# Kernel tuning notes

Hardware: AMD Instinct MI355X
Metric: run time of the kernel (lower is better)

Reference implementation:

```python
import jax, jax.numpy as jnp
import numpy as np

B, L, C_IN, D, H, DFF, NL, NC, PH = 32, 512, 16, 512, 8, 2048, 3, 10, 128
DH = D // H


def circ_conv1d(x, w):
    # x: [B, C, S] with circular padding 1 on spatial dim, w: [O, C, 3]
    xp = jnp.concatenate([x[..., -1:], x, x[..., :1]], axis=-1)
    return jax.lax.conv_general_dilated(xp, w, (1,), 'VALID',
                                        dimension_numbers=('NCH', 'OIH', 'NCH'))


def positional_embedding(length, d):
    pos = jnp.arange(length, dtype=jnp.float32)[:, None]
    div = jnp.exp(jnp.arange(0, d, 2, dtype=jnp.float32) * (-np.log(10000.0) / d))
    pe = jnp.zeros((length, d), jnp.float32)
    pe = pe.at[:, 0::2].set(jnp.sin(pos * div))
    pe = pe.at[:, 1::2].set(jnp.cos(pos * div))
    return pe


def layer_norm(x, g, b):
    m = jnp.mean(x, -1, keepdims=True)
    v = jnp.var(x, -1, keepdims=True)
    return (x - m) / jnp.sqrt(v + 1e-5) * g + b


def projector(x, stats, conv_w, w0, b0, w1, b1, w2):
    # x: [B, L, C_IN] (channels = seq_len, spatial = enc_in), stats: [B, 1, C_IN]
    y = circ_conv1d(x, conv_w)                     # [B, 1, C_IN]
    y = jnp.concatenate([y, stats], axis=1)        # [B, 2, C_IN]
    y = y.reshape(x.shape[0], -1)                  # [B, 2*C_IN]
    h = jax.nn.relu(y @ w0.T + b0)
    h = jax.nn.relu(h @ w1.T + b1)
    return h @ w2.T                                # no bias on output


def setup_inputs() -> dict:
    key = jax.random.key(0)
    ks = iter(jax.random.split(key, 64))
    rn = lambda shape, s=0.02: jax.random.normal(next(ks), shape, jnp.float32) * s
    inp = {
        'x_enc': jax.random.normal(next(ks), (B, L, C_IN), jnp.float32),
        'x_mark_enc': jnp.ones((B, L), jnp.float32),
        'tok_w': rn((D, C_IN, 3)),
        'Wq': rn((NL, D, D)), 'bq': jnp.zeros((NL, D)),
        'Wk': rn((NL, D, D)), 'bk': jnp.zeros((NL, D)),
        'Wv': rn((NL, D, D)), 'bv': jnp.zeros((NL, D)),
        'Wo': rn((NL, D, D)), 'bo': jnp.zeros((NL, D)),
        'W1': rn((NL, DFF, D)), 'b1': jnp.zeros((NL, DFF)),
        'W2': rn((NL, D, DFF)), 'b2': jnp.zeros((NL, D)),
        'ln1_g': jnp.ones((NL, D)), 'ln1_b': jnp.zeros((NL, D)),
        'ln2_g': jnp.ones((NL, D)), 'ln2_b': jnp.zeros((NL, D)),
        'norm_g': jnp.ones((D,)), 'norm_b': jnp.zeros((D,)),
        'proj_w': rn((NC, D * L)), 'proj_b': jnp.zeros((NC,)),
        'tau_conv_w': rn((1, L, 3)), 'tau_w0': rn((PH, 2 * C_IN)), 'tau_b0': jnp.zeros((PH,)),
        'tau_w1': rn((PH, PH)), 'tau_b1': jnp.zeros((PH,)), 'tau_w2': rn((1, PH)),
        'del_conv_w': rn((1, L, 3)), 'del_w0': rn((PH, 2 * C_IN)), 'del_b0': jnp.zeros((PH,)),
        'del_w1': rn((PH, PH)), 'del_b1': jnp.zeros((PH,)), 'del_w2': rn((L, PH)),
    }
    return inp


def reference(x_enc, x_mark_enc, tok_w,
              Wq, bq, Wk, bk, Wv, bv, Wo, bo,
              W1, b1, W2, b2, ln1_g, ln1_b, ln2_g, ln2_b,
              norm_g, norm_b, proj_w, proj_b,
              tau_conv_w, tau_w0, tau_b0, tau_w1, tau_b1, tau_w2,
              del_conv_w, del_w0, del_b0, del_w1, del_b1, del_w2):
    # De-stationary statistics (detached in the original)
    x_raw = jax.lax.stop_gradient(x_enc)
    mean_enc = jnp.mean(x_raw, 1, keepdims=True)                 # [B,1,C]
    std_enc = jnp.sqrt(jnp.var(x_raw, 1, keepdims=True) + 1e-5)  # [B,1,C]
    tau = jnp.exp(projector(x_raw, std_enc, tau_conv_w, tau_w0, tau_b0,
                            tau_w1, tau_b1, tau_w2))             # [B,1]
    delta = projector(x_raw, mean_enc, del_conv_w, del_w0, del_b0,
                      del_w1, del_b1, del_w2)                    # [B,L]

    # DataEmbedding: circular token conv + sinusoidal positional encoding
    tok = circ_conv1d(jnp.transpose(x_enc, (0, 2, 1)), tok_w)    # [B,D,L]
    x = jnp.transpose(tok, (0, 2, 1)) + positional_embedding(L, D)[None]

    scale = 1.0 / np.sqrt(DH)
    tau4 = tau.reshape(B, 1, 1, 1)
    delta4 = delta[:, None, None, :]
    for i in range(NL):
        q = (x @ Wq[i].T + bq[i]).reshape(B, L, H, DH)
        k = (x @ Wk[i].T + bk[i]).reshape(B, L, H, DH)
        v = (x @ Wv[i].T + bv[i]).reshape(B, L, H, DH)
        scores = jnp.einsum('blhe,bshe->bhls', q, k) * tau4 + delta4
        A = jax.nn.softmax(scale * scores, axis=-1)
        o = jnp.einsum('bhls,bshd->blhd', A, v).reshape(B, L, D)
        o = o @ Wo[i].T + bo[i]
        x = layer_norm(x + o, ln1_g[i], ln1_b[i])
        y = jax.nn.gelu(x @ W1[i].T + b1[i], approximate=False) @ W2[i].T + b2[i]
        x = layer_norm(x + y, ln2_g[i], ln2_b[i])
    x = layer_norm(x, norm_g, norm_b)

    out = jax.nn.gelu(x, approximate=False)
    out = out * x_mark_enc[..., None]
    out = out.reshape(B, -1) @ proj_w.T + proj_b                 # [B, NC]
    return out
```

## Files before the change

kernel.cpp:

```cpp
#include <hip/hip_runtime.h>
#include <hip/hip_bf16.h>
#include <cstdint>

#define DEVINL __device__ __forceinline__

typedef unsigned short u16;
typedef short bf16x8 __attribute__((ext_vector_type(8)));
typedef float f32x4 __attribute__((ext_vector_type(4)));

DEVINL u16 f2b(float f) {
    union { float f; uint32_t u; } x{f};
    uint32_t r = x.u + 0x7fffu + ((x.u >> 16) & 1u);
    return (u16)(r >> 16);
}
DEVINL float b2f(u16 h) {
    union { uint32_t u; float f; } x{(uint32_t)h << 16};
    return x.f;
}
DEVINL float gelu_exact(float v) {
    return 0.5f * v * (1.0f + erff(v * 0.70710678118654752f));
}
DEVINL void gload_lds16(const void* g, void* l) {
    __builtin_amdgcn_global_load_lds(
        (const __attribute__((address_space(1))) void*)(uintptr_t)g,
        (__attribute__((address_space(3))) void*)(uint32_t)(uintptr_t)l,
        16, 0, 0);
}

__global__ void f2b_kernel(const float* __restrict__ in, u16* __restrict__ out, int n) {
    int i = (blockIdx.x * 256 + threadIdx.x) * 8;
    if (i + 8 <= n) {
        float4 a = *(const float4*)(in + i);
        float4 b = *(const float4*)(in + i + 4);
        u16 t[8] = {f2b(a.x), f2b(a.y), f2b(a.z), f2b(a.w),
                    f2b(b.x), f2b(b.y), f2b(b.z), f2b(b.w)};
        *(uint4*)(out + i) = *(const uint4*)t;
    }
}

__global__ void packb_kernel(const float* __restrict__ bq, const float* __restrict__ bk,
                             const float* __restrict__ bv, float* __restrict__ out) {
    int idx = blockIdx.x * 256 + threadIdx.x;
    if (idx >= 3 * 1536) return;
    int i = idx / 1536, j = idx - i * 1536;
    float v = (j < 512) ? bq[i * 512 + j]
            : (j < 1024) ? bk[i * 512 + j - 512]
                         : bv[i * 512 + j - 1024];
    out[idx] = v;
}

__global__ void pe_kernel(float* __restrict__ pet) {
    int l = blockIdx.x, d2 = threadIdx.x;
    float freq = expf(-(float)(2 * d2) * 0.0179889460390f);
    float ang = (float)l * freq;
    pet[l * 512 + 2 * d2]     = sinf(ang);
    pet[l * 512 + 2 * d2 + 1] = cosf(ang);
}

__global__ void stats_kernel(const float* __restrict__ xe, float* __restrict__ mean,
                             float* __restrict__ stdv) {
    int b = blockIdx.x, ln = threadIdx.x;
    int c = ln & 15, part = ln >> 4;
    float s = 0.f, sq = 0.f;
    for (int l = part; l < 512; l += 4) {
        float x = xe[(size_t)b * 8192 + l * 16 + c];
        s += x; sq += x * x;
    }
    s += __shfl_xor(s, 16);  s += __shfl_xor(s, 32);
    sq += __shfl_xor(sq, 16); sq += __shfl_xor(sq, 32);
    if (part == 0) {
        float m = s * (1.0f / 512.0f);
        mean[b * 16 + c] = m;
        stdv[b * 16 + c] = sqrtf(sq * (1.0f / 512.0f) - m * m + 1e-5f);
    }
}

__global__ __launch_bounds__(128)
void proj_kernel(const float* __restrict__ xe, const float* __restrict__ stats,
                 const float* __restrict__ cw, const float* __restrict__ w0,
                 const float* __restrict__ b0, const float* __restrict__ w1,
                 const float* __restrict__ b1, const float* __restrict__ w2,
                 float* __restrict__ outp, int outn, int do_exp) {
    __shared__ float zl[32], h0l[128], h1l[128], red[2];
    int b = blockIdx.x, tid = threadIdx.x;
    {
        int c = tid >> 3, part = tid & 7;
        float acc = 0.f;
        for (int l = part; l < 512; l += 8) {
            const float* xr = xe + (size_t)b * 8192 + l * 16;
            float w0v = cw[l * 3 + 0], w1v = cw[l * 3 + 1], w2v = cw[l * 3 + 2];
            acc += xr[(c + 15) & 15] * w0v + xr[c] * w1v + xr[(c + 1) & 15] * w2v;
        }
        acc += __shfl_xor(acc, 1); acc += __shfl_xor(acc, 2); acc += __shfl_xor(acc, 4);
        if (part == 0) zl[c] = acc;
        if (tid < 16) zl[16 + tid] = stats[b * 16 + tid];
    }
    __syncthreads();
    {
        float acc = b0[tid];
        #pragma unroll
        for (int i = 0; i < 32; ++i) acc += zl[i] * w0[tid * 32 + i];
        h0l[tid] = fmaxf(acc, 0.0f);
    }
    __syncthreads();
    {
        float acc = b1[tid];
        for (int i = 0; i < 128; ++i) acc += h0l[i] * w1[tid * 128 + i];
        h1l[tid] = fmaxf(acc, 0.0f);
    }
    __syncthreads();
    if (outn == 1) {
        float p = h1l[tid] * w2[tid];
        p += __shfl_xor(p, 1);  p += __shfl_xor(p, 2);  p += __shfl_xor(p, 4);
        p += __shfl_xor(p, 8);  p += __shfl_xor(p, 16); p += __shfl_xor(p, 32);
        if ((tid & 63) == 0) red[tid >> 6] = p;
        __syncthreads();
        if (tid == 0) {
            float v = red[0] + red[1];
            outp[b] = do_exp ? expf(v) : v;
        }
    } else {
        for (int l = tid; l < outn; l += 128) {
            float acc = 0.f;
            for (int i = 0; i < 128; ++i) acc += h1l[i] * w2[l * 128 + i];
            outp[(size_t)b * outn + l] = acc;
        }
    }
}

__global__ __launch_bounds__(256)
void tokconv_kernel(const float* __restrict__ xe, const float* __restrict__ tw,
                    const float* __restrict__ pet,
                    float* __restrict__ xf, u16* __restrict__ xb) {
    __shared__ float xs[34][16];
    int lt = blockIdx.x, b = blockIdx.y, tid = threadIdx.x;
    int l0 = lt * 32;
    for (int idx = tid; idx < 34 * 16; idx += 256) {
        int r = idx >> 4, c = idx & 15;
        int gl = (l0 - 1 + r + 512) & 511;
        xs[r][c] = xe[(size_t)b * 8192 + gl * 16 + c];
    }
    __syncthreads();
    for (int dd = tid; dd < 512; dd += 256) {
        float twr[48];
        #pragma unroll
        for (int i = 0; i < 48; ++i) twr[i] = tw[dd * 48 + i];
        for (int l = 0; l < 32; ++l) {
            float acc = 0.f;
            #pragma unroll
            for (int c = 0; c < 16; ++c) {
                acc += xs[l][c]     * twr[c * 3 + 0];
                acc += xs[l + 1][c] * twr[c * 3 + 1];
                acc += xs[l + 2][c] * twr[c * 3 + 2];
            }
            float vv = acc + pet[(size_t)(l0 + l) * 512 + dd];
            size_t idx = ((size_t)b * 512 + l0 + l) * 512 + dd;
            xf[idx] = vv;
            xb[idx] = f2b(vv);
        }
    }
}

template <int ACT, int OBF>
__global__ __launch_bounds__(256)
void gemm_bt(const u16* __restrict__ A, const u16* __restrict__ B,
             const float* __restrict__ bias, void* __restrict__ Cv0,
             u16* __restrict__ Cv1, int M, int N, int K, int Kc) {
    __shared__ u16 smem[3][2][128 * 32];
    const int tid = threadIdx.x, wv = tid >> 6, ln = tid & 63;
    const int nwg = gridDim.x * gridDim.y;
    const int bid = blockIdx.y * gridDim.x + blockIdx.x;
    const int wg  = (bid & 7) * (nwg >> 3) + (bid >> 3);
    const int n0 = (wg % gridDim.x) * 128;
    const int m0 = (wg / gridDim.x) * 128;
    const int kz = blockIdx.z;
    const int wm = (wv >> 1) * 64, wn = (wv & 1) * 64;
    const int lo = ln & 15, hi = ln >> 4;
    f32x4 acc[4][4] = {};
    const int r0 = wv * 16 + (ln >> 2);
    const int sl = ln & 3;
    const int k0 = kz * Kc;

    auto stage = [&](int buf, int kt) {
        #pragma unroll
        for (int c = 0; c < 2; ++c) {
            int row = r0 + c * 64;
            int ssl = sl ^ ((row >> 1) & 3);
            int ldsoff = row * 32 + sl * 8;
            gload_lds16(A + (size_t)(m0 + row) * K + kt + ssl * 8, (char*)smem[buf][0] + ldsoff * 2);
            gload_lds16(B + (size_t)(n0 + row) * K + kt + ssl * 8, (char*)smem[buf][1] + ldsoff * 2);
        }
    };

    const int nt = Kc >> 5;
    stage(0, k0);
    if (nt > 1) stage(1, k0 + 32);
    for (int t = 0; t < nt; ++t) {
        if (t + 1 < nt) { asm volatile("s_waitcnt vmcnt(4)" ::: "memory"); }
        else            { asm volatile("s_waitcnt vmcnt(0)" ::: "memory"); }
        __builtin_amdgcn_s_barrier();
        if (t + 2 < nt) stage((t + 2) % 3, k0 + (t + 2) * 32);
        const u16* As = smem[t % 3][0];
        const u16* Bs = smem[t % 3][1];
        bf16x8 af[4], bfr[4];
        #pragma unroll
        for (int i = 0; i < 4; ++i) {
            int row = wm + i * 16 + lo;
            int slot = hi ^ ((row >> 1) & 3);
            af[i] = *(const bf16x8*)(As + row * 32 + slot * 8);
        }
        #pragma unroll
        for (int j = 0; j < 4; ++j) {
            int row = wn + j * 16 + lo;
            int slot = hi ^ ((row >> 1) & 3);
            bfr[j] = *(const bf16x8*)(Bs + row * 32 + slot * 8);
        }
        #pragma unroll
        for (int i = 0; i < 4; ++i)
            #pragma unroll
            for (int j = 0; j < 4; ++j)
                acc[i][j] = __builtin_amdgcn_mfma_f32_16x16x32_bf16(af[i], bfr[j], acc[i][j], 0, 0, 0);
    }
    __syncthreads();

    const bool second = (kz != 0);
    float* ep = (float*)smem + wv * (16 * 68);
    #pragma unroll
    for (int i = 0; i < 4; ++i) {
        #pragma unroll
        for (int j = 0; j < 4; ++j) {
            int col = n0 + wn + j * 16 + lo;
            float bv = second ? 0.0f : bias[col];
            #pragma unroll
            for (int r = 0; r < 4; ++r) {
                float v = acc[i][j][r] + bv;
                if (ACT == 1 && !second) v = gelu_exact(v);
                ep[(hi * 4 + r) * 68 + j * 16 + lo] = v;
            }
        }
        #pragma unroll
        for (int pp = 0; pp < 4; ++pp) {
            int rl = pp * 4 + hi;
            float4 vv = *(const float4*)(ep + rl * 68 + lo * 4);
            size_t row = (size_t)(m0 + wm + i * 16 + rl);
            int col = n0 + wn + lo * 4;
            if (second) {
                u16 t4[4] = {f2b(vv.x), f2b(vv.y), f2b(vv.z), f2b(vv.w)};
                *(uint2*)(Cv1 + row * N + col) = *(const uint2*)t4;
            } else if (OBF) {
                u16 t4[4] = {f2b(vv.x), f2b(vv.y), f2b(vv.z), f2b(vv.w)};
                *(uint2*)((u16*)Cv0 + row * N + col) = *(const uint2*)t4;
            } else {
                *(float4*)((float*)Cv0 + row * N + col) = vv;
            }
        }
    }
}

__global__ __launch_bounds__(512)
void attn2_kernel(const u16* __restrict__ qkv, const float* __restrict__ tau,
                  const float* __restrict__ delta, u16* __restrict__ o) {
    __shared__ u16 KL[64 * 64];
    __shared__ u16 VT[64 * 72];
    __shared__ u16 PL[8][32 * 64];
    const int tid = threadIdx.x, w = tid >> 6, ln = tid & 63;
    const int lo = ln & 15, hi = ln >> 4;
    const int qh = blockIdx.x, h = blockIdx.y, b = blockIdx.z;
    const size_t qrow0 = (size_t)b * 512;
    const u16* qp = qkv;
    const u16* kp = qkv + 512;
    const u16* vp = qkv + 1024;
    const int hofs = h * 64;
    const float ts = tau[b] * 0.125f;
    u16* Pw = (u16*)PL[w];
    const int q0 = qh * 256 + w * 32;

    bf16x8 qa[2][2];
    #pragma unroll
    for (int i = 0; i < 2; ++i)
        #pragma unroll
        for (int ks = 0; ks < 2; ++ks)
            qa[i][ks] = *(const bf16x8*)(qp + (qrow0 + q0 + i * 16 + lo) * 1536 + hofs + ks * 32 + hi * 8);

    float m_run[2] = {-1e30f, -1e30f};
    float l_run[2] = {0.f, 0.f};
    f32x4 oacc[2][4] = {};

    const int vsl = tid & 7, vsr = tid >> 3;
    uint4 vreg = *(const uint4*)(vp + (qrow0 + vsr) * 1536 + hofs + vsl * 8);

    for (int nt = 0; nt < 8; ++nt) {
        __syncthreads();
        {
            int s = tid >> 3, j = tid & 7;
            int jl = j ^ (s & 7);
            gload_lds16(kp + (qrow0 + nt * 64 + s) * 1536 + hofs + jl * 8,
                        (char*)KL + tid * 16);
        }
        {
            u16 tmp[8]; *(uint4*)tmp = vreg;
            #pragma unroll
            for (int e = 0; e < 8; ++e) {
                int d = vsl * 8 + e;
                int byt = d * 144 + (((vsr >> 3) ^ vsl) << 4) + (vsr & 7) * 2;
                *(u16*)((char*)VT + byt) = tmp[e];
            }
        }
        if (nt < 7)
            vreg = *(const uint4*)(vp + (qrow0 + (nt + 1) * 64 + vsr) * 1536 + hofs + vsl * 8);
        __syncthreads();

        f32x4 sacc[2][4] = {};
        #pragma unroll
        for (int ks = 0; ks < 2; ++ks) {
            #pragma unroll
            for (int jn = 0; jn < 4; ++jn) {
                int s = jn * 16 + lo;
                int phys = (ks * 4 + hi) ^ (s & 7);
                bf16x8 kb = *(const bf16x8*)((const char*)KL + s * 128 + phys * 16);
                #pragma unroll
                for (int i = 0; i < 2; ++i)
                    sacc[i][jn] = __builtin_amdgcn_mfma_f32_16x16x32_bf16(kb, qa[i][ks], sacc[i][jn], 0, 0, 0);
            }
        }
        float tmax[2] = {-1e30f, -1e30f};
        #pragma unroll
        for (int jn = 0; jn < 4; ++jn) {
            float4 dv4 = *(const float4*)(delta + b * 512 + nt * 64 + jn * 16 + hi * 4);
            float dv[4] = {dv4.x, dv4.y, dv4.z, dv4.w};
            #pragma unroll
            for (int i = 0; i < 2; ++i)
                #pragma unroll
                for (int r = 0; r < 4; ++r) {
                    float v = sacc[i][jn][r] * ts + dv[r] * 0.125f;
                    sacc[i][jn][r] = v;
                    tmax[i] = fmaxf(tmax[i], v);
                }
        }
        #pragma unroll
        for (int i = 0; i < 2; ++i) {
            tmax[i] = fmaxf(tmax[i], __shfl_xor(tmax[i], 16));
            tmax[i] = fmaxf(tmax[i], __shfl_xor(tmax[i], 32));
            float mnew = fmaxf(m_run[i], tmax[i]);
            float fac = __expf(m_run[i] - mnew);
            m_run[i] = mnew;
            l_run[i] *= fac;
            #pragma unroll
            for (int jd = 0; jd < 4; ++jd)
                #pragma unroll
                for (int r = 0; r < 4; ++r) oacc[i][jd][r] *= fac;
        }
        #pragma unroll
        for (int i = 0; i < 2; ++i) {
            float ls = 0.f;
            #pragma unroll
            for (int jn = 0; jn < 4; ++jn) {
                float p0 = __expf(sacc[i][jn][0] - m_run[i]);
                float p1 = __expf(sacc[i][jn][1] - m_run[i]);
                float p2 = __expf(sacc[i][jn][2] - m_run[i]);
                float p3 = __expf(sacc[i][jn][3] - m_run[i]);
                ls += (p0 + p1) + (p2 + p3);
                uint2 pk;
                pk.x = (uint32_t)f2b(p0) | ((uint32_t)f2b(p1) << 16);
                pk.y = (uint32_t)f2b(p2) | ((uint32_t)f2b(p3) << 16);
                int q = i * 16 + lo;
                int ls16 = jn * 2 + (hi >> 1);
                int byt = q * 128 + (((ls16 ^ (q & 7)) << 4)) + (hi & 1) * 8;
                *(uint2*)((char*)Pw + byt) = pk;
            }
            ls += __shfl_xor(ls, 16);
            ls += __shfl_xor(ls, 32);
            l_run[i] += ls;
        }
        #pragma unroll
        for (int ks2 = 0; ks2 < 2; ++ks2) {
            bf16x8 pa[2];
            #pragma unroll
            for (int i = 0; i < 2; ++i) {
                int q = i * 16 + lo;
                int phys = (ks2 * 4 + hi) ^ (q & 7);
                pa[i] = *(const bf16x8*)((const char*)Pw + q * 128 + phys * 16);
            }
            #pragma unroll
            for (int jd = 0; jd < 4; ++jd) {
                int d = jd * 16 + lo;
                int cs = (ks2 * 4 + hi) ^ ((d >> 3) & 7);
                bf16x8 vb = *(const bf16x8*)((const char*)VT + d * 144 + cs * 16);
                #pragma unroll
                for (int i = 0; i < 2; ++i)
                    oacc[i][jd] = __builtin_amdgcn_mfma_f32_16x16x32_bf16(vb, pa[i], oacc[i][jd], 0, 0, 0);
            }
        }
    }
    #pragma unroll
    for (int i = 0; i < 2; ++i) {
        float inv = 1.0f / l_run[i];
        #pragma unroll
        for (int jd = 0; jd < 4; ++jd) {
            u16 t4[4];
            #pragma unroll
            for (int r = 0; r < 4; ++r) t4[r] = f2b(oacc[i][jd][r] * inv);
            size_t row = qrow0 + q0 + i * 16 + lo;
            *(uint2*)(o + row * 512 + hofs + jd * 16 + hi * 4) = *(const uint2*)t4;
        }
    }
}

__global__ __launch_bounds__(256)
void ln3_kernel(const float* __restrict__ xin, const float* __restrict__ res0,
                const u16* res1, const float* __restrict__ g,
                const float* __restrict__ bta,
                float* __restrict__ xout, u16* xbf) {
    const int row = blockIdx.x * 4 + (threadIdx.x >> 6);
    const int ln = threadIdx.x & 63;
    const float* xr = xin + (size_t)row * 512;
    const float* rr = res0 + (size_t)row * 512;
    const u16* pr = res1 + (size_t)row * 512;
    float4 a = *(const float4*)(xr + ln * 4);
    float4 c = *(const float4*)(xr + 256 + ln * 4);
    float4 ra = *(const float4*)(rr + ln * 4);
    float4 rc = *(const float4*)(rr + 256 + ln * 4);
    uint2 pa_ = *(const uint2*)(pr + ln * 4);
    uint2 pc_ = *(const uint2*)(pr + 256 + ln * 4);
    const u16* pa16 = (const u16*)&pa_;
    const u16* pc16 = (const u16*)&pc_;
    a.x += ra.x + b2f(pa16[0]); a.y += ra.y + b2f(pa16[1]);
    a.z += ra.z + b2f(pa16[2]); a.w += ra.w + b2f(pa16[3]);
    c.x += rc.x + b2f(pc16[0]); c.y += rc.y + b2f(pc16[1]);
    c.z += rc.z + b2f(pc16[2]); c.w += rc.w + b2f(pc16[3]);
    float s = a.x + a.y + a.z + a.w + c.x + c.y + c.z + c.w;
    float sq = a.x*a.x + a.y*a.y + a.z*a.z + a.w*a.w + c.x*c.x + c.y*c.y + c.z*c.z + c.w*c.w;
    #pragma unroll
    for (int m = 1; m < 64; m <<= 1) { s += __shfl_xor(s, m); sq += __shfl_xor(sq, m); }
    float mean = s * 0.001953125f;
    float var = sq * 0.001953125f - mean * mean;
    float rstd = rsqrtf(var + 1e-5f);
    float4 g0 = *(const float4*)(g + ln * 4);
    float4 g1 = *(const float4*)(g + 256 + ln * 4);
    float4 b0 = *(const float4*)(bta + ln * 4);
    float4 b1 = *(const float4*)(bta + 256 + ln * 4);
    float4 o0, o1;
    o0.x = (a.x - mean) * rstd * g0.x + b0.x;
    o0.y = (a.y - mean) * rstd * g0.y + b0.y;
    o0.z = (a.z - mean) * rstd * g0.z + b0.z;
    o0.w = (a.w - mean) * rstd * g0.w + b0.w;
    o1.x = (c.x - mean) * rstd * g1.x + b1.x;
    o1.y = (c.y - mean) * rstd * g1.y + b1.y;
    o1.z = (c.z - mean) * rstd * g1.z + b1.z;
    o1.w = (c.w - mean) * rstd * g1.w + b1.w;
    *(float4*)(xout + (size_t)row * 512 + ln * 4) = o0;
    *(float4*)(xout + (size_t)row * 512 + 256 + ln * 4) = o1;
    u16 t0[4] = {f2b(o0.x), f2b(o0.y), f2b(o0.z), f2b(o0.w)};
    u16 t1[4] = {f2b(o1.x), f2b(o1.y), f2b(o1.z), f2b(o1.w)};
    *(uint2*)(xbf + (size_t)row * 512 + ln * 4) = *(const uint2*)t0;
    *(uint2*)(xbf + (size_t)row * 512 + 256 + ln * 4) = *(const uint2*)t1;
}

__global__ __launch_bounds__(256)
void lngelu_kernel(const float* __restrict__ xin, const float* __restrict__ g,
                   const float* __restrict__ bta, const float* __restrict__ mark,
                   u16* __restrict__ outb) {
    const int row = blockIdx.x * 4 + (threadIdx.x >> 6);
    const int ln = threadIdx.x & 63;
    const float* xr = xin + (size_t)row * 512;
    float4 a = *(const float4*)(xr + ln * 4);
    float4 c = *(const float4*)(xr + 256 + ln * 4);
    float s = a.x + a.y + a.z + a.w + c.x + c.y + c.z + c.w;
    float sq = a.x*a.x + a.y*a.y + a.z*a.z + a.w*a.w + c.x*c.x + c.y*c.y + c.z*c.z + c.w*c.w;
    #pragma unroll
    for (int m = 1; m < 64; m <<= 1) { s += __shfl_xor(s, m); sq += __shfl_xor(sq, m); }
    float mean = s * 0.001953125f;
    float var = sq * 0.001953125f - mean * mean;
    float rstd = rsqrtf(var + 1e-5f);
    float mk = mark[row];
    float4 g0 = *(const float4*)(g + ln * 4);
    float4 g1 = *(const float4*)(g + 256 + ln * 4);
    float4 b0 = *(const float4*)(bta + ln * 4);
    float4 b1 = *(const float4*)(bta + 256 + ln * 4);
    float v0 = gelu_exact((a.x - mean) * rstd * g0.x + b0.x) * mk;
    float v1 = gelu_exact((a.y - mean) * rstd * g0.y + b0.y) * mk;
    float v2 = gelu_exact((a.z - mean) * rstd * g0.z + b0.z) * mk;
    float v3 = gelu_exact((a.w - mean) * rstd * g0.w + b0.w) * mk;
    float v4 = gelu_exact((c.x - mean) * rstd * g1.x + b1.x) * mk;
    float v5 = gelu_exact((c.y - mean) * rstd * g1.y + b1.y) * mk;
    float v6 = gelu_exact((c.z - mean) * rstd * g1.z + b1.z) * mk;
    float v7 = gelu_exact((c.w - mean) * rstd * g1.w + b1.w) * mk;
    u16 t0[4] = {f2b(v0), f2b(v1), f2b(v2), f2b(v3)};
    u16 t1[4] = {f2b(v4), f2b(v5), f2b(v6), f2b(v7)};
    *(uint2*)(outb + (size_t)row * 512 + ln * 4) = *(const uint2*)t0;
    *(uint2*)(outb + (size_t)row * 512 + 256 + ln * 4) = *(const uint2*)t1;
}

__global__ __launch_bounds__(256)
void fproj_kernel(const u16* __restrict__ gb, const u16* __restrict__ pw,
                  const float* __restrict__ pb, float* __restrict__ out) {
    __shared__ float red[32][4];
    int n = blockIdx.x, ks = blockIdx.y, tid = threadIdx.x;
    float acc[32];
    #pragma unroll
    for (int m = 0; m < 32; ++m) acc[m] = 0.f;
    for (int j = 0; j < 8; ++j) {
        size_t k0 = (size_t)ks * 16384 + j * 2048 + tid * 8;
        bf16x8 w8 = *(const bf16x8*)(pw + (size_t)n * 262144 + k0);
        float wf[8];
        #pragma unroll
        for (int e = 0; e < 8; ++e) wf[e] = b2f((u16)w8[e]);
        #pragma unroll
        for (int m = 0; m < 32; ++m) {
            bf16x8 g8 = *(const bf16x8*)(gb + (size_t)m * 262144 + k0);
            float a = acc[m];
            #pragma unroll
            for (int e = 0; e < 8; ++e) a += b2f((u16)g8[e]) * wf[e];
            acc[m] = a;
        }
    }
    int w = tid >> 6;
    #pragma unroll
    for (int m = 0; m < 32; ++m) {
        float s = acc[m];
        s += __shfl_xor(s, 1);  s += __shfl_xor(s, 2);  s += __shfl_xor(s, 4);
        s += __shfl_xor(s, 8);  s += __shfl_xor(s, 16); s += __shfl_xor(s, 32);
        if ((tid & 63) == 0) red[m][w] = s;
    }
    __syncthreads();
    if (tid < 32) {
        int m = tid;
        float s = red[m][0] + red[m][1] + red[m][2] + red[m][3];
        if (ks == 0) s += pb[n];
        atomicAdd(&out[m * 10 + n], s);
    }
}

extern "C" void kernel_launch(void* const* d_in, const int* in_sizes, int n_in,
                              void* d_out, int out_size, void* d_ws, size_t ws_size,
                              hipStream_t stream) {
    const float* x_enc  = (const float*)d_in[0];
    const float* x_mark = (const float*)d_in[1];
    const float* tok_w  = (const float*)d_in[2];
    const float* Wq = (const float*)d_in[3];   const float* bq = (const float*)d_in[4];
    const float* Wk = (const float*)d_in[5];   const float* bk = (const float*)d_in[6];
    const float* Wv = (const float*)d_in[7];   const float* bv = (const float*)d_in[8];
    const float* Wo = (const float*)d_in[9];   const float* bo = (const float*)d_in[10];
    const float* W1 = (const float*)d_in[11];  const float* b1 = (const float*)d_in[12];
    const float* W2 = (const float*)d_in[13];  const float* b2 = (const float*)d_in[14];
    const float* ln1_g = (const float*)d_in[15]; const float* ln1_b = (const float*)d_in[16];
    const float* ln2_g = (const float*)d_in[17]; const float* ln2_b = (const float*)d_in[18];
    const float* norm_g = (const float*)d_in[19]; const float* norm_b = (const float*)d_in[20];
    const float* proj_w = (const float*)d_in[21]; const float* proj_b = (const float*)d_in[22];
    const float* tau_cw = (const float*)d_in[23];
    const float* tau_w0 = (const float*)d_in[24]; const float* tau_b0 = (const float*)d_in[25];
    const float* tau_w1 = (const float*)d_in[26]; const float* tau_b1 = (const float*)d_in[27];
    const float* tau_w2 = (const float*)d_in[28];
    const float* del_cw = (const float*)d_in[29];
    const float* del_w0 = (const float*)d_in[30]; const float* del_b0 = (const float*)d_in[31];
    const float* del_w1 = (const float*)d_in[32]; const float* del_b1 = (const float*)d_in[33];
    const float* del_w2 = (const float*)d_in[34];
    float* out = (float*)d_out;

    char* ws = (char*)d_ws;
    size_t off = 0;
    auto alloc = [&](size_t bytes) -> void* {
        void* p = ws + off;
        off += (bytes + 255) & ~(size_t)255;
        return p;
    };
    u16* wqkvb = (u16*)alloc((size_t)3 * 786432 * 2);
    u16* wob = (u16*)alloc(786432 * 2);
    u16* w1b = (u16*)alloc(3145728 * 2);
    u16* w2b = (u16*)alloc(3145728 * 2);
    u16* pwb = (u16*)alloc(2621440 * 2);
    float* bqkvb = (float*)alloc(3 * 1536 * 4);
    float* petab = (float*)alloc((size_t)262144 * 4);
    float* meanb = (float*)alloc(512 * 4);
    float* stdb  = (float*)alloc(512 * 4);
    float* taub  = (float*)alloc(32 * 4);
    float* delb  = (float*)alloc(16384 * 4);
    float* xf = (float*)alloc((size_t)8388608 * 4);
    u16*  xb  = (u16*)alloc((size_t)8388608 * 2);
    float* sf = (float*)alloc((size_t)8388608 * 4);
    u16* qkvb = (u16*)alloc((size_t)16384 * 1536 * 2);
    u16* ob   = (u16*)alloc((size_t)8388608 * 2);
    u16* hb   = qkvb;
    u16* gbuf = qkvb;
    u16* p1o  = qkvb;
    u16* p1f  = xb;

    auto cvt = [&](const float* src, u16* dst, int n) {
        f2b_kernel<<<dim3((n + 2047) / 2048), dim3(256), 0, stream>>>(src, dst, n);
    };
    for (int i = 0; i < 3; ++i) {
        cvt(Wq + (size_t)i * 262144, wqkvb + (size_t)i * 786432 + 0,      262144);
        cvt(Wk + (size_t)i * 262144, wqkvb + (size_t)i * 786432 + 262144, 262144);
        cvt(Wv + (size_t)i * 262144, wqkvb + (size_t)i * 786432 + 524288, 262144);
    }
    cvt(Wo, wob, 786432);
    cvt(W1, w1b, 3145728); cvt(W2, w2b, 3145728);
    cvt(proj_w, pwb, 2621440);
    packb_kernel<<<dim3(18), dim3(256), 0, stream>>>(bq, bk, bv, bqkvb);
    pe_kernel<<<dim3(512), dim3(256), 0, stream>>>(petab);

    stats_kernel<<<dim3(32), dim3(64), 0, stream>>>(x_enc, meanb, stdb);
    proj_kernel<<<dim3(32), dim3(128), 0, stream>>>(x_enc, stdb, tau_cw, tau_w0, tau_b0,
                                                    tau_w1, tau_b1, tau_w2, taub, 1, 1);
    proj_kernel<<<dim3(32), dim3(128), 0, stream>>>(x_enc, meanb, del_cw, del_w0, del_b0,
                                                    del_w1, del_b1, del_w2, delb, 512, 0);
    tokconv_kernel<<<dim3(16, 32), dim3(256), 0, stream>>>(x_enc, tok_w, petab, xf, xb);

    for (int i = 0; i < 3; ++i) {
        const u16* wqkv_i = wqkvb + (size_t)i * 786432;
        const u16* wo_i = wob + (size_t)i * 262144;
        const u16* w1_i = w1b + (size_t)i * 1048576;
        const u16* w2_i = w2b + (size_t)i * 1048576;
        gemm_bt<0, 1><<<dim3(12, 128, 1), dim3(256), 0, stream>>>(
            xb, wqkv_i, bqkvb + i * 1536, qkvb, nullptr, 16384, 1536, 512, 512);
        attn2_kernel<<<dim3(2, 8, 32), dim3(512), 0, stream>>>(qkvb, taub, delb, ob);
        gemm_bt<0, 0><<<dim3(4, 128, 2), dim3(256), 0, stream>>>(
            ob, wo_i, bo + i * 512, sf, p1o, 16384, 512, 512, 256);
        ln3_kernel<<<dim3(4096), dim3(256), 0, stream>>>(xf, sf, p1o,
            ln1_g + i * 512, ln1_b + i * 512, xf, xb);
        gemm_bt<1, 1><<<dim3(16, 128, 1), dim3(256), 0, stream>>>(
            xb, w1_i, b1 + i * 2048, hb, nullptr, 16384, 2048, 512, 512);
        gemm_bt<0, 0><<<dim3(4, 128, 2), dim3(256), 0, stream>>>(
            hb, w2_i, b2 + i * 512, sf, p1f, 16384, 512, 2048, 1024);
        ln3_kernel<<<dim3(4096), dim3(256), 0, stream>>>(xf, sf, p1f,
            ln2_g + i * 512, ln2_b + i * 512, xf, xb);
    }

    lngelu_kernel<<<dim3(4096), dim3(256), 0, stream>>>(xf, norm_g, norm_b, x_mark, gbuf);
    hipMemsetAsync(d_out, 0, (size_t)out_size * 4, stream);
    fproj_kernel<<<dim3(10, 16), dim3(256), 0, stream>>>(gbuf, pwb, proj_b, out);
}
```

Before: 1.001 ms.

## Switch GEMMs to 32x32x16 MFMA, bf16 split-K partials, fuse weight conversions

The GEMM kernel now uses 32x32x16 bf16 MFMA tiles (2x2 per wave) instead of 16x16x32, which reduces LDS fragment reads per MFMA. The first split-K partial is also stored as bf16 instead of fp32, halving that buffer's traffic into the layernorm kernel at some precision cost. The many per-tensor weight conversion launches are merged into two kernels to cut launch overhead. The memory clobbers on the waitcnt asm were also dropped, which risks compiler reordering around the LDS pipeline.

```diff
diff --git a/kernel.cpp b/kernel.cpp
--- a/kernel.cpp
+++ b/kernel.cpp
@@ -7,6 +7,7 @@
 typedef unsigned short u16;
 typedef short bf16x8 __attribute__((ext_vector_type(8)));
 typedef float f32x4 __attribute__((ext_vector_type(4)));
+typedef float f32x16 __attribute__((ext_vector_type(16)));
 
 DEVINL u16 f2b(float f) {
     union { float f; uint32_t u; } x{f};
@@ -26,16 +27,38 @@
         (__attribute__((address_space(3))) void*)(uint32_t)(uintptr_t)l,
         16, 0, 0);
 }
-
-__global__ void f2b_kernel(const float* __restrict__ in, u16* __restrict__ out, int n) {
-    int i = (blockIdx.x * 256 + threadIdx.x) * 8;
-    if (i + 8 <= n) {
-        float4 a = *(const float4*)(in + i);
-        float4 b = *(const float4*)(in + i + 4);
-        u16 t[8] = {f2b(a.x), f2b(a.y), f2b(a.z), f2b(a.w),
-                    f2b(b.x), f2b(b.y), f2b(b.z), f2b(b.w)};
-        *(uint4*)(out + i) = *(const uint4*)t;
-    }
+DEVINL void cvt8(const float* src, u16* dst) {
+    float4 a = *(const float4*)src;
+    float4 b = *(const float4*)(src + 4);
+    u16 t[8] = {f2b(a.x), f2b(a.y), f2b(a.z), f2b(a.w),
+                f2b(b.x), f2b(b.y), f2b(b.z), f2b(b.w)};
+    *(uint4*)dst = *(const uint4*)t;
+}
+
+__global__ __launch_bounds__(256)
+void cvtqkv_kernel(const float* __restrict__ Wq, const float* __restrict__ Wk,
+                   const float* __restrict__ Wv, u16* __restrict__ dst) {
+    size_t i = ((size_t)blockIdx.x * 256 + threadIdx.x) * 8;
+    int slice = (int)(i >> 18);
+    int layer = slice / 3, which = slice - layer * 3;
+    size_t rem = i & 262143;
+    const float* src = (which == 0 ? Wq : which == 1 ? Wk : Wv) + (size_t)layer * 262144 + rem;
+    u16* d = dst + (size_t)layer * 786432 + (size_t)which * 262144 + rem;
+    cvt8(src, d);
+}
+__global__ __launch_bounds__(256)
+void cvt4_kernel(const float* __restrict__ s0, const float* __restrict__ s1,
+                 const float* __restrict__ s2, const float* __restrict__ s3,
+                 u16* __restrict__ d0, u16* __restrict__ d1,
+                 u16* __restrict__ d2, u16* __restrict__ d3) {
+    size_t i = ((size_t)blockIdx.x * 256 + threadIdx.x) * 8;
+    if (i < 786432) { cvt8(s0 + i, d0 + i); return; }
+    i -= 786432;
+    if (i < 3145728) { cvt8(s1 + i, d1 + i); return; }
+    i -= 3145728;
+    if (i < 3145728) { cvt8(s2 + i, d2 + i); return; }
+    i -= 3145728;
+    if (i < 2621440) { cvt8(s3 + i, d3 + i); }
 }
 
 __global__ void packb_kernel(const float* __restrict__ bq, const float* __restrict__ bk,
@@ -161,11 +184,11 @@
     }
 }
 
-template <int ACT, int OBF>
+template <int ACT>
 __global__ __launch_bounds__(256)
-void gemm_bt(const u16* __restrict__ A, const u16* __restrict__ B,
-             const float* __restrict__ bias, void* __restrict__ Cv0,
-             u16* __restrict__ Cv1, int M, int N, int K, int Kc) {
+void gemm32(const u16* __restrict__ A, const u16* __restrict__ B,
+            const float* __restrict__ bias, u16* __restrict__ Cv0,
+            u16* __restrict__ Cv1, int M, int N, int K, int Kc) {
     __shared__ u16 smem[3][2][128 * 32];
     const int tid = threadIdx.x, wv = tid >> 6, ln = tid & 63;
     const int nwg = gridDim.x * gridDim.y;
@@ -175,16 +198,16 @@
     const int m0 = (wg / gridDim.x) * 128;
     const int kz = blockIdx.z;
     const int wm = (wv >> 1) * 64, wn = (wv & 1) * 64;
-    const int lo = ln & 15, hi = ln >> 4;
-    f32x4 acc[4][4] = {};
-    const int r0 = wv * 16 + (ln >> 2);
+    const int l31 = ln & 31, h2 = ln >> 5;
+    f32x16 acc[2][2] = {};
+    const int r0s = wv * 16 + (ln >> 2);
     const int sl = ln & 3;
     const int k0 = kz * Kc;
 
     auto stage = [&](int buf, int kt) {
         #pragma unroll
         for (int c = 0; c < 2; ++c) {
-            int row = r0 + c * 64;
+            int row = r0s + c * 64;
             int ssl = sl ^ ((row >> 1) & 3);
             int ldsoff = row * 32 + sl * 8;
             gload_lds16(A + (size_t)(m0 + row) * K + kt + ssl * 8, (char*)smem[buf][0] + ldsoff * 2);
@@ -196,63 +219,73 @@
     stage(0, k0);
     if (nt > 1) stage(1, k0 + 32);
     for (int t = 0; t < nt; ++t) {
-        if (t + 1 < nt) { asm volatile("s_waitcnt vmcnt(4)" ::: "memory"); }
-        else            { asm volatile("s_waitcnt vmcnt(0)" ::: "memory"); }
+        if (t + 1 < nt) { asm volatile("s_waitcnt vmcnt(4)"); }
+        else            { asm volatile("s_waitcnt vmcnt(0)"); }
         __builtin_amdgcn_s_barrier();
         if (t + 2 < nt) stage((t + 2) % 3, k0 + (t + 2) * 32);
         const u16* As = smem[t % 3][0];
         const u16* Bs = smem[t % 3][1];
-        bf16x8 af[4], bfr[4];
-        #pragma unroll
-        for (int i = 0; i < 4; ++i) {
-            int row = wm + i * 16 + lo;
-            int slot = hi ^ ((row >> 1) & 3);
-            af[i] = *(const bf16x8*)(As + row * 32 + slot * 8);
-        }
-        #pragma unroll
-        for (int j = 0; j < 4; ++j) {
-            int row = wn + j * 16 + lo;
-            int slot = hi ^ ((row >> 1) & 3);
-            bfr[j] = *(const bf16x8*)(Bs + row * 32 + slot * 8);
-        }
-        #pragma unroll
-        for (int i = 0; i < 4; ++i)
-            #pragma unroll
-            for (int j = 0; j < 4; ++j)
-                acc[i][j] = __builtin_amdgcn_mfma_f32_16x16x32_bf16(af[i], bfr[j], acc[i][j], 0, 0, 0);
+        bf16x8 af[2][2], bfr[2][2];
+        #pragma unroll
+        for (int mi = 0; mi < 2; ++mi) {
+            int row = wm + mi * 32 + l31;
+            int swz = (row >> 1) & 3;
+            #pragma unroll
+            for (int kk = 0; kk < 2; ++kk) {
+                int phys = (kk * 2 + h2) ^ swz;
+                af[mi][kk] = *(const bf16x8*)(As + row * 32 + phys * 8);
+            }
+        }
+        #pragma unroll
+        for (int nj = 0; nj < 2; ++nj) {
+            int row = wn + nj * 32 + l31;
+            int swz = (row >> 1) & 3;
+            #pragma unroll
+            for (int kk = 0; kk < 2; ++kk) {
+                int phys = (kk * 2 + h2) ^ swz;
+                bfr[nj][kk] = *(const bf16x8*)(Bs + row * 32 + phys * 8);
+            }
+        }
+        #pragma unroll
+        for (int mi = 0; mi < 2; ++mi)
+            #pragma unroll
+            for (int nj = 0; nj < 2; ++nj)
+                #pragma unroll
+                for (int kk = 0; kk < 2; ++kk)
+                    acc[mi][nj] = __builtin_amdgcn_mfma_f32_32x32x16_bf16(
+                        af[mi][kk], bfr[nj][kk], acc[mi][nj], 0, 0, 0);
     }
     __syncthreads();
 
     const bool second = (kz != 0);
-    float* ep = (float*)smem + wv * (16 * 68);
+    float* eps = (float*)smem + wv * (16 * 68);
+    u16* Cout = second ? Cv1 : Cv0;
     #pragma unroll
-    for (int i = 0; i < 4; ++i) {
-        #pragma unroll
-        for (int j = 0; j < 4; ++j) {
-            int col = n0 + wn + j * 16 + lo;
-            float bv = second ? 0.0f : bias[col];
-            #pragma unroll
-            for (int r = 0; r < 4; ++r) {
-                float v = acc[i][j][r] + bv;
-                if (ACT == 1 && !second) v = gelu_exact(v);
-                ep[(hi * 4 + r) * 68 + j * 16 + lo] = v;
-            }
+    for (int ch = 0; ch < 4; ++ch) {
+        const int mi = ch >> 1, rsel = ch & 1;
+        #pragma unroll
+        for (int nj = 0; nj < 2; ++nj) {
+            int col = nj * 32 + l31;
+            float bv = second ? 0.0f : bias[n0 + wn + col];
+            #pragma unroll
+            for (int r1l = 0; r1l < 2; ++r1l)
+                #pragma unroll
+                for (int rr = 0; rr < 4; ++rr) {
+                    int reg = rr + 4 * (rsel * 2 + r1l);
+                    int rloc = h2 * 4 + rr + 8 * r1l;
+                    float v = acc[mi][nj][reg] + bv;
+                    if (ACT == 1 && !second) v = gelu_exact(v);
+                    eps[rloc * 68 + col] = v;
+                }
         }
         #pragma unroll
         for (int pp = 0; pp < 4; ++pp) {
-            int rl = pp * 4 + hi;
-            float4 vv = *(const float4*)(ep + rl * 68 + lo * 4);
-            size_t row = (size_t)(m0 + wm + i * 16 + rl);
-            int col = n0 + wn + lo * 4;
-            if (second) {
-                u16 t4[4] = {f2b(vv.x), f2b(vv.y), f2b(vv.z), f2b(vv.w)};
-                *(uint2*)(Cv1 + row * N + col) = *(const uint2*)t4;
-            } else if (OBF) {
-                u16 t4[4] = {f2b(vv.x), f2b(vv.y), f2b(vv.z), f2b(vv.w)};
-                *(uint2*)((u16*)Cv0 + row * N + col) = *(const uint2*)t4;
-            } else {
-                *(float4*)((float*)Cv0 + row * N + col) = vv;
-            }
+            int rl = pp * 4 + (ln >> 4);
+            float4 vv = *(const float4*)(eps + rl * 68 + (ln & 15) * 4);
+            size_t row = (size_t)(m0 + wm + ch * 16 + rl);
+            int col = n0 + wn + (ln & 15) * 4;
+            u16 t4[4] = {f2b(vv.x), f2b(vv.y), f2b(vv.z), f2b(vv.w)};
+            *(uint2*)(Cout + row * N + col) = *(const uint2*)t4;
         }
     }
 }
@@ -407,27 +440,27 @@
 }
 
 __global__ __launch_bounds__(256)
-void ln3_kernel(const float* __restrict__ xin, const float* __restrict__ res0,
+void ln3_kernel(const float* __restrict__ xin, const u16* res0,
                 const u16* res1, const float* __restrict__ g,
                 const float* __restrict__ bta,
                 float* __restrict__ xout, u16* xbf) {
     const int row = blockIdx.x * 4 + (threadIdx.x >> 6);
     const int ln = threadIdx.x & 63;
     const float* xr = xin + (size_t)row * 512;
-    const float* rr = res0 + (size_t)row * 512;
-    const u16* pr = res1 + (size_t)row * 512;
+    const u16* r0p = res0 + (size_t)row * 512;
+    const u16* r1p = res1 + (size_t)row * 512;
     float4 a = *(const float4*)(xr + ln * 4);
     float4 c = *(const float4*)(xr + 256 + ln * 4);
-    float4 ra = *(const float4*)(rr + ln * 4);
-    float4 rc = *(const float4*)(rr + 256 + ln * 4);
-    uint2 pa_ = *(const uint2*)(pr + ln * 4);
-    uint2 pc_ = *(const uint2*)(pr + 256 + ln * 4);
-    const u16* pa16 = (const u16*)&pa_;
-    const u16* pc16 = (const u16*)&pc_;
-    a.x += ra.x + b2f(pa16[0]); a.y += ra.y + b2f(pa16[1]);
-    a.z += ra.z + b2f(pa16[2]); a.w += ra.w + b2f(pa16[3]);
-    c.x += rc.x + b2f(pc16[0]); c.y += rc.y + b2f(pc16[1]);
-    c.z += rc.z + b2f(pc16[2]); c.w += rc.w + b2f(pc16[3]);
+    uint2 qa_ = *(const uint2*)(r0p + ln * 4);
+    uint2 qc_ = *(const uint2*)(r0p + 256 + ln * 4);
+    uint2 pa_ = *(const uint2*)(r1p + ln * 4);
+    uint2 pc_ = *(const uint2*)(r1p + 256 + ln * 4);
+    const u16* qa16 = (const u16*)&qa_;  const u16* qc16 = (const u16*)&qc_;
+    const u16* pa16 = (const u16*)&pa_;  const u16* pc16 = (const u16*)&pc_;
+    a.x += b2f(qa16[0]) + b2f(pa16[0]); a.y += b2f(qa16[1]) + b2f(pa16[1]);
+    a.z += b2f(qa16[2]) + b2f(pa16[2]); a.w += b2f(qa16[3]) + b2f(pa16[3]);
+    c.x += b2f(qc16[0]) + b2f(pc16[0]); c.y += b2f(qc16[1]) + b2f(pc16[1]);
+    c.z += b2f(qc16[2]) + b2f(pc16[2]); c.w += b2f(qc16[3]) + b2f(pc16[3]);
     float s = a.x + a.y + a.z + a.w + c.x + c.y + c.z + c.w;
     float sq = a.x*a.x + a.y*a.y + a.z*a.z + a.w*a.w + c.x*c.x + c.y*c.y + c.z*c.z + c.w*c.w;
     #pragma unroll
@@ -577,7 +610,7 @@
     float* delb  = (float*)alloc(16384 * 4);
     float* xf = (float*)alloc((size_t)8388608 * 4);
     u16*  xb  = (u16*)alloc((size_t)8388608 * 2);
-    float* sf = (float*)alloc((size_t)8388608 * 4);
+    u16*  sfb = (u16*)alloc((size_t)8388608 * 2);
     u16* qkvb = (u16*)alloc((size_t)16384 * 1536 * 2);
     u16* ob   = (u16*)alloc((size_t)8388608 * 2);
     u16* hb   = qkvb;
@@ -585,17 +618,8 @@
     u16* p1o  = qkvb;
     u16* p1f  = xb;
 
-    auto cvt = [&](const float* src, u16* dst, int n) {
-        f2b_kernel<<<dim3((n + 2047) / 2048), dim3(256), 0, stream>>>(src, dst, n);
-    };
-    for (int i = 0; i < 3; ++i) {
-        cvt(Wq + (size_t)i * 262144, wqkvb + (size_t)i * 786432 + 0,      262144);
-        cvt(Wk + (size_t)i * 262144, wqkvb + (size_t)i * 786432 + 262144, 262144);
-        cvt(Wv + (size_t)i * 262144, wqkvb + (size_t)i * 786432 + 524288, 262144);
-    }
-    cvt(Wo, wob, 786432);
-    cvt(W1, w1b, 3145728); cvt(W2, w2b, 3145728);
-    cvt(proj_w, pwb, 2621440);
+    cvtqkv_kernel<<<dim3(1152), dim3(256), 0, stream>>>(Wq, Wk, Wv, wqkvb);
+    cvt4_kernel<<<dim3(5030), dim3(256), 0, stream>>>(Wo, W1, W2, proj_w, wob, w1b, w2b, pwb);
     packb_kernel<<<dim3(18), dim3(256), 0, stream>>>(bq, bk, bv, bqkvb);
     pe_kernel<<<dim3(512), dim3(256), 0, stream>>>(petab);
 
@@ -611,18 +635,18 @@
         const u16* wo_i = wob + (size_t)i * 262144;
         const u16* w1_i = w1b + (size_t)i * 1048576;
         const u16* w2_i = w2b + (size_t)i * 1048576;
-        gemm_bt<0, 1><<<dim3(12, 128, 1), dim3(256), 0, stream>>>(
+        gemm32<0><<<dim3(12, 128, 1), dim3(256), 0, stream>>>(
             xb, wqkv_i, bqkvb + i * 1536, qkvb, nullptr, 16384, 1536, 512, 512);
         attn2_kernel<<<dim3(2, 8, 32), dim3(512), 0, stream>>>(qkvb, taub, delb, ob);
-        gemm_bt<0, 0><<<dim3(4, 128, 2), dim3(256), 0, stream>>>(
-            ob, wo_i, bo + i * 512, sf, p1o, 16384, 512, 512, 256);
-        ln3_kernel<<<dim3(4096), dim3(256), 0, stream>>>(xf, sf, p1o,
+        gemm32<0><<<dim3(4, 128, 2), dim3(256), 0, stream>>>(
+            ob, wo_i, bo + i * 512, sfb, p1o, 16384, 512, 512, 256);
+        ln3_kernel<<<dim3(4096), dim3(256), 0, stream>>>(xf, sfb, p1o,
             ln1_g + i * 512, ln1_b + i * 512, xf, xb);
-        gemm_bt<1, 1><<<dim3(16, 128, 1), dim3(256), 0, stream>>>(
+        gemm32<1><<<dim3(16, 128, 1), dim3(256), 0, stream>>>(
             xb, w1_i, b1 + i * 2048, hb, nullptr, 16384, 2048, 512, 512);
-        gemm_bt<0, 0><<<dim3(4, 128, 2), dim3(256), 0, stream>>>(
-            hb, w2_i, b2 + i * 512, sf, p1f, 16384, 512, 2048, 1024);
-        ln3_kernel<<<dim3(4096), dim3(256), 0, stream>>>(xf, sf, p1f,
+        gemm32<0><<<dim3(4, 128, 2), dim3(256), 0, stream>>>(
+            hb, w2_i, b2 + i * 512, sfb, p1f, 16384, 512, 2048, 1024);
+        ln3_kernel<<<dim3(4096), dim3(256), 0, stream>>>(xf, sfb, p1f,
             ln2_g + i * 512, ln2_b + i * 512, xf, xb);
     }
 
```

After: 980.8 us. -2.1%, faster.
